# Kernel tuning notes

Hardware: AMD Instinct MI355X
Metric: run time of the kernel (lower is better)

The kernel has to match this reference:

```python
import jax, jax.numpy as jnp
import numpy as np

D_QKV = 64

def setup_inputs() -> dict:
    key = jax.random.key(0)
    k1, k2, k3, k4 = jax.random.split(key, 4)
    B, T, D = 4, 2048, 1024
    x = jax.random.normal(k1, (B, T, D), dtype=jnp.float32)
    Wq = jax.random.normal(k2, (D, D_QKV), dtype=jnp.float32) * (D ** -0.5)
    Wk = jax.random.normal(k3, (D, D_QKV), dtype=jnp.float32) * (D ** -0.5)
    Wv = jax.random.normal(k4, (D, D_QKV), dtype=jnp.float32) * (D ** -0.5)
    return {"x": x, "Wq": Wq, "Wk": Wk, "Wv": Wv}

def reference(x, Wq, Wk, Wv):
    # x: [B, T, D]; single-head causal attention with head dim d_qkv
    T = x.shape[1]
    q = jnp.einsum("btd,de->bte", x, Wq)  # [B, T, d]
    k = jnp.einsum("btd,de->bte", x, Wk)
    v = jnp.einsum("btd,de->bte", x, Wv)
    scores = jnp.einsum("bqe,bke->bqk", q, k) / (D_QKV ** 0.5)  # [B, T, T]
    causal = jnp.tril(jnp.ones((T, T), dtype=bool))
    scores = jnp.where(causal, scores, -jnp.inf)
    attn = jax.nn.softmax(scores, axis=2)
    return jnp.einsum("bqk,bke->bqe", attn, v)  # [B, T, d]
```

## Files before the change

### kernel.cpp

```cpp
#include <hip/hip_runtime.h>
#include <hip/hip_bf16.h>
#include <math.h>

typedef __hip_bfloat16 bf16;
typedef __bf16 bf16x8 __attribute__((ext_vector_type(8)));
typedef float f32x4 __attribute__((ext_vector_type(4)));
typedef unsigned short u16x8 __attribute__((ext_vector_type(8)));

#define B_SZ   4
#define T_SEQ  2048
#define D_IN   1024
#define D_QKV  64
#define BT     (B_SZ * T_SEQ)
#define PSTR   72
#define TOTW   2112
#define ANB    512

#define GLD_LDS(gp, lp) __builtin_amdgcn_global_load_lds(                     \
    (const __attribute__((address_space(1))) void*)(gp),                      \
    (__attribute__((address_space(3))) void*)(lp), 16, 0, 0)

__global__ __launch_bounds__(256) void wt_prep(
    const float* __restrict__ Wq, const float* __restrict__ Wk,
    const float* __restrict__ Wv, bf16* __restrict__ wt)
{
    __shared__ float ws[64 * 65];
    const int bx = blockIdx.x;
    const int m  = bx >> 4;
    const int k0 = (bx & 15) << 6;
    const float* W = (m == 0) ? Wq : (m == 1) ? Wk : Wv;
    const int tid = threadIdx.x;
    #pragma unroll
    for (int i = 0; i < 16; ++i) {
        const int idx = i * 256 + tid;
        const int kk = idx >> 6, nn = idx & 63;
        ws[kk * 65 + nn] = W[(size_t)(k0 + kk) * D_QKV + nn];
    }
    __syncthreads();
    const int n = tid >> 2, kq = (tid & 3) << 4;
    bf16 tmp[16];
    #pragma unroll
    for (int j = 0; j < 16; ++j)
        tmp[j] = __float2bfloat16(ws[(kq + j) * 65 + n]);
    uint4* dst = (uint4*)(wt + (size_t)(m * 64 + n) * D_IN + k0 + kq);
    dst[0] = ((uint4*)tmp)[0];
    dst[1] = ((uint4*)tmp)[1];
}

__global__ __launch_bounds__(256) void qkv_proj_mfma(
    const float* __restrict__ x, const bf16* __restrict__ wt,
    bf16* __restrict__ qb, bf16* __restrict__ kb, bf16* __restrict__ vt)
{
    __shared__ uint4 As[2][256];
    __shared__ uint4 Bs[2][1536];

    const int tid  = threadIdx.x;
    const int wave = tid >> 6;
    const int lane = tid & 63;
    const int col  = lane & 15;
    const int quad = lane >> 4;
    const int m0   = blockIdx.x * 16;

    f32x4 acc[3];
    #pragma unroll
    for (int i = 0; i < 3; ++i) acc[i] = (f32x4){0.f, 0.f, 0.f, 0.f};

    auto stage = [&](int it, int buf) {
        const int k0 = it * 64;
        #pragma unroll
        for (int j = 0; j < 7; ++j) {
            const int s = wave + j * 4;
            if (s < 4) {
                const int c = s * 64 + lane;
                const int r = c >> 4;
                const int ccl = ((c & 15) - r) & 15;
                const float* g = x + (size_t)(m0 + r) * D_IN + k0 + ccl * 4;
                GLD_LDS(g, &As[buf][s * 64]);
            } else {
                const int bs = s - 4;
                const int c = bs * 64 + lane;
                const int n = c >> 3;
                const int ccl = ((c & 7) - n) & 7;
                const bf16* g = wt + (size_t)n * D_IN + k0 + ccl * 8;
                GLD_LDS(g, &Bs[buf][bs * 64]);
            }
        }
    };

    stage(0, 0);
    const int r = col;
    #pragma unroll 1
    for (int it = 0; it < 16; ++it) {
        __syncthreads();
        if (it + 1 < 16) stage(it + 1, (it + 1) & 1);
        const float4* Ac = (const float4*)As[it & 1];
        const uint4*  Bc = Bs[it & 1];
        #pragma unroll
        for (int s = 0; s < 2; ++s) {
            const int ca = s * 8 + quad * 2;
            const float4 a0 = Ac[r * 16 + ((ca + r) & 15)];
            const float4 a1 = Ac[r * 16 + ((ca + 1 + r) & 15)];
            const bf16x8 af = (bf16x8){(__bf16)a0.x, (__bf16)a0.y, (__bf16)a0.z, (__bf16)a0.w,
                                       (__bf16)a1.x, (__bf16)a1.y, (__bf16)a1.z, (__bf16)a1.w};
            #pragma unroll
            for (int i = 0; i < 3; ++i) {
                const int n = wave * 48 + i * 16 + col;
                const bf16x8 bfr = __builtin_bit_cast(bf16x8,
                    Bc[n * 8 + ((s * 4 + quad + n) & 7)]);
                acc[i] = __builtin_amdgcn_mfma_f32_16x16x32_bf16(af, bfr, acc[i], 0, 0, 0);
            }
        }
    }

    const int bb = m0 >> 11;
    const int tl = m0 & (T_SEQ - 1);
    #pragma unroll
    for (int i = 0; i < 3; ++i) {
        const int n = wave * 48 + i * 16 + col;
        #pragma unroll
        for (int rr = 0; rr < 4; ++rr) {
            const int row = m0 + quad * 4 + rr;
            const bf16 vq = __float2bfloat16(acc[i][rr]);
            if (n < 64)       qb[(size_t)row * D_QKV + n] = vq;
            else if (n < 128) kb[(size_t)row * D_QKV + (n - 64)] = vq;
            else              vt[(size_t)bb * D_QKV * T_SEQ + (size_t)(n - 128) * T_SEQ
                                 + (tl + quad * 4 + rr)] = vq;
        }
    }
}

__global__ __launch_bounds__(256) void attn_kernel(
    const bf16* __restrict__ qb, const bf16* __restrict__ kb,
    const bf16* __restrict__ vt, float* __restrict__ Op, float* __restrict__ lp)
{
    __shared__ uint4 Ks[2][512];
    __shared__ uint4 Vs[2][512];
    __shared__ unsigned short plds[4 * 16 * PSTR];

    const int tid  = threadIdx.x;
    const int wave = tid >> 6;
    const int lane = tid & 63;
    const int col  = lane & 15;
    const int quad = lane >> 4;
    const int bx   = blockIdx.x;

    const int lo = (bx * 33) >> 3;
    const int hi = ((bx + 1) * 33) >> 3;
    const int items = hi - lo;

    int b = lo / 528;
    int rres = lo - b * 528;
    int t = (int)((sqrtf(8.f * (float)rres + 1.f) - 1.f) * 0.5f);
    while ((t + 1) * (t + 2) / 2 <= rres) ++t;
    while (t * (t + 1) / 2 > rres) --t;
    int c = rres - t * (t + 1) / 2;

    unsigned short* pl = plds + wave * 16 * PSTR;
    const u16x8* p8 = (const u16x8*)pl;

    auto stage = [&](int sb, int sc, int buf) {
        const bf16* kbp = kb + (size_t)sb * T_SEQ * D_QKV;
        const bf16* vtp = vt + (size_t)sb * D_QKV * T_SEQ;
        const int kb0 = sc * 64;
        #pragma unroll
        for (int j = 0; j < 4; ++j) {
            const int s = wave + j * 4;
            if (s < 8) {
                const int ch = s * 64 + lane;
                const int key = ch >> 3;
                const int ccl = ((ch & 7) - key) & 7;
                const bf16* g = kbp + (size_t)(kb0 + key) * D_QKV + ccl * 8;
                GLD_LDS(g, &Ks[buf][s * 64]);
            } else {
                const int vs = s - 8;
                const int ch = vs * 64 + lane;
                const int d = ch >> 3;
                const int ccl = ((ch & 7) - d) & 7;
                const bf16* g = vtp + (size_t)d * T_SEQ + kb0 + ccl * 8;
                GLD_LDS(g, &Vs[buf][vs * 64]);
            }
        }
    };

    stage(b, c, 0);

    bf16x8 aq0, aq1;
    f32x4 o[4];
    float ls[4];
    int segw = lo;

    #pragma unroll 1
    for (int i = 0; i < items; ++i) {
        if (i == 0 || c == 0) {
            const uint4* q4 = (const uint4*)(qb + (size_t)b * T_SEQ * D_QKV);
            const int qrow = t * 64 + wave * 16 + col;
            aq0 = __builtin_bit_cast(bf16x8, q4[qrow * 8 + quad]);
            aq1 = __builtin_bit_cast(bf16x8, q4[qrow * 8 + 4 + quad]);
            #pragma unroll
            for (int dt = 0; dt < 4; ++dt) o[dt] = (f32x4){0.f, 0.f, 0.f, 0.f};
            #pragma unroll
            for (int rr = 0; rr < 4; ++rr) ls[rr] = 0.f;
            segw = lo + i;
        }

        int nb = b, nt = t, nc = c + 1;
        if (nc > t) { nc = 0; ++nt; if (nt == 32) { nt = 0; ++nb; } }

        __syncthreads();
        if (i + 1 < items) stage(nb, nc, (i + 1) & 1);
        const uint4* Kc = Ks[i & 1];
        const uint4* Vc = Vs[i & 1];

        f32x4 sc4[4];
        #pragma unroll
        for (int nt2 = 0; nt2 < 4; ++nt2) {
            const int kp = nt2 * 16 + col;
            const bf16x8 bk0 = __builtin_bit_cast(bf16x8, Kc[kp * 8 + ((quad + kp) & 7)]);
            const bf16x8 bk1 = __builtin_bit_cast(bf16x8, Kc[kp * 8 + ((4 + quad + kp) & 7)]);
            sc4[nt2] = (f32x4){0.f, 0.f, 0.f, 0.f};
            sc4[nt2] = __builtin_amdgcn_mfma_f32_16x16x32_bf16(aq0, bk0, sc4[nt2], 0, 0, 0);
            sc4[nt2] = __builtin_amdgcn_mfma_f32_16x16x32_bf16(aq1, bk1, sc4[nt2], 0, 0, 0);
        }

        if (c == t) {
            #pragma unroll
            for (int nt2 = 0; nt2 < 4; ++nt2) {
                const int kp = c * 64 + nt2 * 16 + col;
                #pragma unroll
                for (int rr = 0; rr < 4; ++rr)
                    if (kp > t * 64 + wave * 16 + quad * 4 + rr) sc4[nt2][rr] = -INFINITY;
            }
        }

        #pragma unroll
        for (int nt2 = 0; nt2 < 4; ++nt2) {
            #pragma unroll
            for (int rr = 0; rr < 4; ++rr) {
                const float pv = __expf(sc4[nt2][rr] * 0.125f);
                ls[rr] += pv;
                pl[(quad * 4 + rr) * PSTR + nt2 * 16 + col] =
                    __builtin_bit_cast(unsigned short, __float2bfloat16(pv));
            }
        }

        const bf16x8 pa0 = __builtin_bit_cast(bf16x8, p8[col * 9 + quad]);
        const bf16x8 pa1 = __builtin_bit_cast(bf16x8, p8[col * 9 + 4 + quad]);

        #pragma unroll
        for (int dt = 0; dt < 4; ++dt) {
            const int dp = dt * 16 + col;
            const bf16x8 bv0 = __builtin_bit_cast(bf16x8, Vc[dp * 8 + ((quad + dp) & 7)]);
            const bf16x8 bv1 = __builtin_bit_cast(bf16x8, Vc[dp * 8 + ((4 + quad + dp) & 7)]);
            o[dt] = __builtin_amdgcn_mfma_f32_16x16x32_bf16(pa0, bv0, o[dt], 0, 0, 0);
            o[dt] = __builtin_amdgcn_mfma_f32_16x16x32_bf16(pa1, bv1, o[dt], 0, 0, 0);
        }

        if (c == t || i == items - 1) {
            float lr[4];
            #pragma unroll
            for (int rr = 0; rr < 4; ++rr) {
                lr[rr] = ls[rr];
                #pragma unroll
                for (int msk = 1; msk < 16; msk <<= 1)
                    lr[rr] += __shfl_xor(lr[rr], msk);
            }
            const int pbase = segw * 64 + wave * 16;
            #pragma unroll
            for (int dt = 0; dt < 4; ++dt)
                #pragma unroll
                for (int rr = 0; rr < 4; ++rr)
                    Op[(size_t)(pbase + quad * 4 + rr) * D_QKV + dt * 16 + col] = o[dt][rr];
            if (col == 0) {
                #pragma unroll
                for (int rr = 0; rr < 4; ++rr)
                    lp[pbase + quad * 4 + rr] = lr[rr];
            }
        }

        b = nb; t = nt; c = nc;
    }
}

__global__ __launch_bounds__(256) void combine_attn(
    const float* __restrict__ Op, const float* __restrict__ lp,
    float* __restrict__ out)
{
    const int idx = blockIdx.x * 256 + threadIdx.x;
    const int qg = idx >> 6, d = idx & 63;
    const int g = qg >> 6, qq = qg & 63;
    const int b = g >> 5, t = g & 31;
    const int W0 = b * 528 + t * (t + 1) / 2;
    float s = 0.f, l = 0.f;
    int prevown = (8 * (W0 - 1) + 7) / 33;
    #pragma unroll 1
    for (int c = 0; c <= t; ++c) {
        const int w = W0 + c;
        const int own = (8 * w + 7) / 33;
        if (c == 0 || own != prevown) {
            s += Op[(size_t)(w * 64 + qq) * D_QKV + d];
            l += lp[w * 64 + qq];
        }
        prevown = own;
    }
    out[(size_t)qg * D_QKV + d] = s / l;
}

extern "C" void kernel_launch(void* const* d_in, const int* in_sizes, int n_in,
                              void* d_out, int out_size, void* d_ws, size_t ws_size,
                              hipStream_t stream) {
    const float* x  = (const float*)d_in[0];
    const float* Wq = (const float*)d_in[1];
    const float* Wk = (const float*)d_in[2];
    const float* Wv = (const float*)d_in[3];
    float* out = (float*)d_out;

    char* ws = (char*)d_ws;
    bf16*  qb = (bf16*)(ws);
    bf16*  kb = (bf16*)(ws + (1u << 20));
    bf16*  vt = (bf16*)(ws + (2u << 20));
    bf16*  wt = (bf16*)(ws + (3u << 20));
    float* Op = (float*)(ws + (4u << 20));
    float* lp = (float*)(ws + (40u << 20));

    wt_prep<<<48, 256, 0, stream>>>(Wq, Wk, Wv, wt);
    qkv_proj_mfma<<<512, 256, 0, stream>>>(x, wt, qb, kb, vt);
    attn_kernel<<<ANB, 256, 0, stream>>>(qb, kb, vt, Op, lp);
    combine_attn<<<2048, 256, 0, stream>>>(Op, lp, out);
}
```

Measured before the change: 109.4 us.

## Deepen async LDS prefetch pipelines with explicit vmcnt waits in projection and attention

The QKV projection now prefetches x tiles three stages ahead in a 4-buffer ring while weight tiles stay double-buffered. The attention kernel moves from double to triple buffering of K/V tiles. Both loops replace __syncthreads with explicit s_waitcnt vmcnt counts plus a bare s_barrier, so loads already in flight need not fully drain each iteration. The aim is to hide global-to-LDS latency behind MFMA work, at the cost of more LDS and fragile hand-counted wait values. In attention a vmcnt(0) is forced at segment starts, presumably because the Q loads there are also vector-memory ops.

New measurement: 110.2 us. Within noise of the previous version (+0.7%).

```diff
diff --git a/kernel.cpp b/kernel.cpp
--- a/kernel.cpp
+++ b/kernel.cpp
@@ -19,6 +19,11 @@
 #define GLD_LDS(gp, lp) __builtin_amdgcn_global_load_lds(                     \
     (const __attribute__((address_space(1))) void*)(gp),                      \
     (__attribute__((address_space(3))) void*)(lp), 16, 0, 0)
+
+#define VMCNT0 asm volatile("s_waitcnt vmcnt(0)" ::: "memory")
+#define VMCNT1 asm volatile("s_waitcnt vmcnt(1)" ::: "memory")
+#define VMCNT2 asm volatile("s_waitcnt vmcnt(2)" ::: "memory")
+#define VMCNT4 asm volatile("s_waitcnt vmcnt(4)" ::: "memory")
 
 __global__ __launch_bounds__(256) void wt_prep(
     const float* __restrict__ Wq, const float* __restrict__ Wk,
@@ -51,7 +56,7 @@
     const float* __restrict__ x, const bf16* __restrict__ wt,
     bf16* __restrict__ qb, bf16* __restrict__ kb, bf16* __restrict__ vt)
 {
-    __shared__ uint4 As[2][256];
+    __shared__ uint4 As[4][256];
     __shared__ uint4 Bs[2][1536];
 
     const int tid  = threadIdx.x;
@@ -65,35 +70,45 @@
     #pragma unroll
     for (int i = 0; i < 3; ++i) acc[i] = (f32x4){0.f, 0.f, 0.f, 0.f};
 
-    auto stage = [&](int it, int buf) {
+    auto stage_A = [&](int it, int buf) {
         const int k0 = it * 64;
-        #pragma unroll
-        for (int j = 0; j < 7; ++j) {
-            const int s = wave + j * 4;
-            if (s < 4) {
-                const int c = s * 64 + lane;
-                const int r = c >> 4;
-                const int ccl = ((c & 15) - r) & 15;
-                const float* g = x + (size_t)(m0 + r) * D_IN + k0 + ccl * 4;
-                GLD_LDS(g, &As[buf][s * 64]);
-            } else {
-                const int bs = s - 4;
-                const int c = bs * 64 + lane;
-                const int n = c >> 3;
-                const int ccl = ((c & 7) - n) & 7;
-                const bf16* g = wt + (size_t)n * D_IN + k0 + ccl * 8;
-                GLD_LDS(g, &Bs[buf][bs * 64]);
-            }
-        }
+        const int s = wave;
+        const int c = s * 64 + lane;
+        const int r = c >> 4;
+        const int ccl = ((c & 15) - r) & 15;
+        const float* g = x + (size_t)(m0 + r) * D_IN + k0 + ccl * 4;
+        GLD_LDS(g, &As[buf][s * 64]);
     };
-
-    stage(0, 0);
+    auto stage_B = [&](int it, int buf) {
+        const int k0 = it * 64;
+        #pragma unroll
+        for (int j = 0; j < 6; ++j) {
+            const int bs = wave + j * 4;
+            const int c = bs * 64 + lane;
+            const int n = c >> 3;
+            const int ccl = ((c & 7) - n) & 7;
+            const bf16* g = wt + (size_t)n * D_IN + k0 + ccl * 8;
+            GLD_LDS(g, &Bs[buf][bs * 64]);
+        }
+    };
+
+    stage_B(0, 0);
+    stage_A(0, 0);
+    stage_A(1, 1);
+    stage_A(2, 2);
+
     const int r = col;
     #pragma unroll 1
     for (int it = 0; it < 16; ++it) {
-        __syncthreads();
-        if (it + 1 < 16) stage(it + 1, (it + 1) & 1);
-        const float4* Ac = (const float4*)As[it & 1];
+        if (it == 0)       VMCNT2;
+        else if (it < 14)  VMCNT1;
+        else               VMCNT0;
+        __builtin_amdgcn_s_barrier();
+
+        if (it + 1 < 16) stage_B(it + 1, (it + 1) & 1);
+        if (it + 3 < 16) stage_A(it + 3, (it + 3) & 3);
+
+        const float4* Ac = (const float4*)As[it & 3];
         const uint4*  Bc = Bs[it & 1];
         #pragma unroll
         for (int s = 0; s < 2; ++s) {
@@ -133,8 +148,8 @@
     const bf16* __restrict__ qb, const bf16* __restrict__ kb,
     const bf16* __restrict__ vt, float* __restrict__ Op, float* __restrict__ lp)
 {
-    __shared__ uint4 Ks[2][512];
-    __shared__ uint4 Vs[2][512];
+    __shared__ uint4 Ks[3][512];
+    __shared__ uint4 Vs[3][512];
     __shared__ unsigned short plds[4 * 16 * PSTR];
 
     const int tid  = threadIdx.x;
@@ -182,7 +197,14 @@
         }
     };
 
+    auto adv = [](int& ab, int& at, int& ac) {
+        if (++ac > at) { ac = 0; if (++at == 32) { at = 0; ++ab; } }
+    };
+
     stage(b, c, 0);
+    int bn = b, tn = t, cn = c;
+    adv(bn, tn, cn);
+    if (items > 1) stage(bn, cn, 1);
 
     bf16x8 aq0, aq1;
     f32x4 o[4];
@@ -191,7 +213,24 @@
 
     #pragma unroll 1
     for (int i = 0; i < items; ++i) {
-        if (i == 0 || c == 0) {
+        const bool segstart = (i == 0 || c == 0);
+
+        if (i == 0) {
+            if (items > 1) VMCNT4; else VMCNT0;
+        } else if (c == 0 || i + 1 >= items) {
+            VMCNT0;
+        } else {
+            VMCNT4;
+        }
+        __builtin_amdgcn_s_barrier();
+
+        if (i + 2 < items) {
+            int b2 = bn, t2 = tn, c2 = cn;
+            adv(b2, t2, c2);
+            stage(b2, c2, (i + 2) % 3);
+        }
+
+        if (segstart) {
             const uint4* q4 = (const uint4*)(qb + (size_t)b * T_SEQ * D_QKV);
             const int qrow = t * 64 + wave * 16 + col;
             aq0 = __builtin_bit_cast(bf16x8, q4[qrow * 8 + quad]);
@@ -203,13 +242,8 @@
             segw = lo + i;
         }
 
-        int nb = b, nt = t, nc = c + 1;
-        if (nc > t) { nc = 0; ++nt; if (nt == 32) { nt = 0; ++nb; } }
-
-        __syncthreads();
-        if (i + 1 < items) stage(nb, nc, (i + 1) & 1);
-        const uint4* Kc = Ks[i & 1];
-        const uint4* Vc = Vs[i & 1];
+        const uint4* Kc = Ks[i % 3];
+        const uint4* Vc = Vs[i % 3];
 
         f32x4 sc4[4];
         #pragma unroll
@@ -277,7 +311,8 @@
             }
         }
 
-        b = nb; t = nt; c = nc;
+        b = bn; t = tn; c = cn;
+        adv(bn, tn, cn);
     }
 }
 
```
